# Performance work log

Measured on AMD Instinct MI355X. Metric: run time of the kernel, lower is better.

Reference implementation:

```python
import jax, jax.numpy as jnp
import numpy as np

EPS = 1e-15


def _cdist(a, b):
    # batched euclidean pairwise distance, a:[B,N,K] b:[B,M,K] -> [B,N,M]
    d2 = (jnp.sum(a * a, -1)[:, :, None] + jnp.sum(b * b, -1)[:, None, :]
          - 2.0 * jnp.einsum('bik,bjk->bij', a, b))
    return jnp.sqrt(jnp.maximum(d2, 0.0))


def _rank3_diag(d_flat):
    # [B,N] -> [B,N,N] diagonal
    eye = jnp.eye(d_flat.shape[1], dtype=d_flat.dtype)
    return eye * d_flat[:, :, None]


def _trace(m):
    return jnp.einsum('bjj->b', m)


def dense_ct_rewiring(x, adj, s, mask):
    s = jnp.tanh(s)
    m = mask[:, :, None].astype(x.dtype)
    x = x * m
    s = s * m
    k = s.shape[-1]
    d_flat = jnp.sum(adj, axis=-1)              # [B,N]
    d = _rank3_diag(d_flat) + EPS               # EPS added to full matrix (faithful to torch)
    L = d - adj
    out_adj = jnp.einsum('bnk,bnm,bml->bkl', s, L, s)
    ct_num = _trace(out_adj)
    ct_den = _trace(jnp.einsum('bnk,bnm,bml->bkl', s, d, s)) + EPS
    ct_dist = _cdist(s, s)                      # [B,N,N]
    vol = _trace(d)                             # [B]
    ct_dist = ct_dist / vol[:, None, None]
    adj_new = ct_dist * adj
    ct_loss = jnp.mean(ct_num / ct_den)
    ss = jnp.einsum('bnk,bnl->bkl', s, s)
    i_s = jnp.eye(k, dtype=ss.dtype)
    ss_n = jnp.sqrt(jnp.sum(ss * ss, axis=(-1, -2), keepdims=True))
    diff = ss / ss_n - i_s
    ortho_loss = jnp.sqrt(jnp.sum(diff * diff))  # global Frobenius norm, mean of scalar
    return adj_new, ct_loss, ortho_loss


def dense_mincut_pool(x, adj, s, mask):
    s = jax.nn.softmax(s, axis=-1)
    m = mask[:, :, None].astype(x.dtype)
    x = x * m
    s = s * m
    k = s.shape[-1]
    out = jnp.einsum('bnk,bnf->bkf', s, x)
    out_adj = jnp.einsum('bnk,bnm,bml->bkl', s, adj, s)
    mincut_num = _trace(out_adj)
    d_flat = jnp.sum(adj, axis=-1) + EPS
    d = _rank3_diag(d_flat)
    mincut_den = _trace(jnp.einsum('bnk,bnm,bml->bkl', s, d, s))
    mincut_loss = jnp.mean(-(mincut_num / mincut_den))
    ss = jnp.einsum('bnk,bnl->bkl', s, s)
    i_s = jnp.eye(k, dtype=ss.dtype)
    ss_n = jnp.sqrt(jnp.sum(ss * ss, axis=(-1, -2), keepdims=True))
    diff = ss / ss_n - i_s / jnp.sqrt(jnp.asarray(float(k), ss.dtype))
    ortho_loss = jnp.mean(jnp.sqrt(jnp.sum(diff * diff, axis=(-1, -2))))
    # zero diagonal, then symmetric degree normalization
    out_adj = out_adj * (1.0 - i_s)
    dk = jnp.sqrt(jnp.sum(out_adj, axis=-1) + EPS) + EPS  # [B,k]
    out_adj = out_adj / dk[:, None, :] / dk[:, :, None]
    return out, out_adj, mincut_loss, ortho_loss


def dense_graph_conv(x, adj, w_rel, b_rel, w_root):
    # PyG DenseGraphConv(aggr='add'): lin_rel(adj @ x) + lin_root(x)
    return jnp.matmul(jnp.matmul(adj, x), w_rel) + b_rel + jnp.matmul(x, w_root)


def ctnet_forward(x, adj, mask,
                  W_lin1, b_lin1, W_pool1, b_pool1, W_pool2, b_pool2,
                  Wrel1, brel1, Wroot1, Wrel2, brel2, Wroot2,
                  W_lin2, b_lin2, W_lin3, b_lin3):
    x = jnp.matmul(x, W_lin1) + b_lin1
    s1 = jnp.matmul(x, W_pool1) + b_pool1
    adj, ct_loss, ortho1 = dense_ct_rewiring(x, adj, s1, mask)
    x = dense_graph_conv(x, adj, Wrel1, brel1, Wroot1)
    s2 = jnp.matmul(x, W_pool2) + b_pool2
    x, adj, mincut2, ortho2 = dense_mincut_pool(x, adj, s2, mask)
    x = dense_graph_conv(x, adj, Wrel2, brel2, Wroot2)
    x = jnp.sum(x, axis=1)
    x = jax.nn.relu(jnp.matmul(x, W_lin2) + b_lin2)
    x = jnp.matmul(x, W_lin3) + b_lin3
    return jax.nn.log_softmax(x, axis=-1), ct_loss + ortho1, mincut2 + ortho2


def _init_lin(key, fan_in, fan_out):
    k1, k2 = jax.random.split(key)
    lim = 1.0 / np.sqrt(fan_in)
    W = jax.random.uniform(k1, (fan_in, fan_out), jnp.float32, -lim, lim)
    b = jax.random.uniform(k2, (fan_out,), jnp.float32, -lim, lim)
    return W, b


def setup_inputs() -> dict:
    key = jax.random.key(0)
    ks = jax.random.split(key, 12)
    B, N, Fin, H, K, OUT, K2 = 16, 1024, 128, 32, 64, 10, 16
    x = jax.random.normal(ks[0], (B, N, Fin), jnp.float32)
    adj = jax.random.uniform(ks[1], (B, N, N), jnp.float32)
    mask = jnp.ones((B, N), jnp.bool_)
    W_lin1, b_lin1 = _init_lin(ks[2], Fin, H)
    W_pool1, b_pool1 = _init_lin(ks[3], H, K)
    W_pool2, b_pool2 = _init_lin(ks[4], H, K2)
    Wrel1, brel1 = _init_lin(ks[5], H, H)
    Wroot1, _ = _init_lin(ks[6], H, H)
    Wrel2, brel2 = _init_lin(ks[7], H, H)
    Wroot2, _ = _init_lin(ks[8], H, H)
    W_lin2, b_lin2 = _init_lin(ks[9], H, H)
    W_lin3, b_lin3 = _init_lin(ks[10], H, OUT)
    return dict(x=x, adj=adj, mask=mask,
                W_lin1=W_lin1, b_lin1=b_lin1, W_pool1=W_pool1, b_pool1=b_pool1,
                W_pool2=W_pool2, b_pool2=b_pool2,
                Wrel1=Wrel1, brel1=brel1, Wroot1=Wroot1,
                Wrel2=Wrel2, brel2=brel2, Wroot2=Wroot2,
                W_lin2=W_lin2, b_lin2=b_lin2, W_lin3=W_lin3, b_lin3=b_lin3)


def reference(x, adj, mask,
              W_lin1, b_lin1, W_pool1, b_pool1, W_pool2, b_pool2,
              Wrel1, brel1, Wroot1, Wrel2, brel2, Wroot2,
              W_lin2, b_lin2, W_lin3, b_lin3):
    return ctnet_forward(x, adj, mask,
                         W_lin1, b_lin1, W_pool1, b_pool1, W_pool2, b_pool2,
                         Wrel1, brel1, Wroot1, Wrel2, brel2, Wroot2,
                         W_lin2, b_lin2, W_lin3, b_lin3)
```

## Files before the change

kernel.cpp:

```cpp
#include <hip/hip_runtime.h>

typedef unsigned short u16;
typedef unsigned int   u32;
typedef __attribute__((ext_vector_type(8))) short bf16x8;
typedef __attribute__((ext_vector_type(4))) float f32x4;

#define EPSF 1e-15f

__device__ __forceinline__ float* accp(float* xb, int b, int a) {
    return xb + (size_t)(b*1024 + a/14)*128 + 114 + (a % 14);
}

__device__ __forceinline__ float bf2f(u16 u) {
    union { u32 i; float f; } v; v.i = ((u32)u) << 16; return v.f;
}
__device__ __forceinline__ u16 f2bf(float f) {
    union { u32 i; float f; } v; v.f = f;
    u32 r = v.i + 0x7fffu + ((v.i >> 16) & 1u);
    return (u16)(r >> 16);
}

__global__ __launch_bounds__(256) void k_a(float* xb,
        const float* __restrict__ W1, const float* __restrict__ b1,
        const float* __restrict__ Wp1, const float* __restrict__ bp1)
{
    __shared__ float W1s[128*32];
    __shared__ float Wp1s[32*64];
    __shared__ float xs[16][128];
    __shared__ float x1s[16][32];
    int tid = threadIdx.x;
    for (int i = tid; i < 1024; i += 256)
        *(float4*)&W1s[i*4] = *(const float4*)&W1[i*4];
    for (int i = tid; i < 512; i += 256)
        *(float4*)&Wp1s[i*4] = *(const float4*)&Wp1[i*4];
    int rbase = blockIdx.x*16;
    for (int e = tid; e < 512; e += 256) {
        int rr = e >> 5, c = e & 31;
        *(float4*)&xs[rr][c*4] = *(const float4*)&xb[(size_t)(rbase + rr)*128 + c*4];
    }
    __syncthreads();
    int w = tid >> 6, l = tid & 63;
    int col = l & 31, half = l >> 5;
    #pragma unroll
    for (int i = 0; i < 4; ++i) {
        int rr = w*4 + i;
        float* xr = xb + (size_t)(rbase + rr)*128;
        if (l == 33) xr[96] = 0.f;
        if (l < 15) xr[113 + l] = 0.f;
        float acc = half ? 0.f : b1[col];
        const float* xrow = &xs[rr][half*64];
        const float* wrow = &W1s[half*64*32 + col];
        for (int f = 0; f < 64; ++f) acc += xrow[f]*wrow[f*32];
        acc += __shfl_down(acc, 32);
        if (l < 32) x1s[rr][l] = acc;
    }
    __syncthreads();
    #pragma unroll
    for (int i = 0; i < 4; ++i) {
        int rr = w*4 + i;
        float* xr = xb + (size_t)(rbase + rr)*128;
        if (l < 32) xr[64 + l] = x1s[rr][l];
        float acc = bp1[l];
        for (int h = 0; h < 32; ++h) acc += x1s[rr][h]*Wp1s[h*64 + l];
        float sv = tanhf(acc);
        u32 me = (u32)f2bf(sv);
        u32 nb = __shfl_down(me, 1);
        if (!(l & 1)) ((u32*)xr)[l >> 1] = me | (nb << 16);
        float svr = bf2f((u16)me);
        float qv = svr*svr;
        for (int off = 32; off; off >>= 1) qv += __shfl_down(qv, off);
        if (l == 0) xr[112] = qv;
    }
}

__global__ __launch_bounds__(256, 6) void k_c(const float* __restrict__ adj, float* xb,
                                              u32* __restrict__ anb)
{
    __shared__ __align__(16) u16 BufB[2][64*72];
    __shared__ __align__(16) float qBs[2][64];
    __shared__ float pw[2][4];
    int tid = threadIdx.x;
    int tjq = blockIdx.x, ti = blockIdx.y, b = blockIdx.z;
    int w = tid >> 6, lane = tid & 63;
    int q = lane >> 4, c16 = lane & 15;
    int rloc = w*16 + c16;
    size_t rowg = (size_t)(b*1024 + ti*64 + rloc);
    const u32* xu = (const u32*)xb;
    float4 a4s[2][4];
    #pragma unroll
    for (int tt = 0; tt < 2; ++tt)
        #pragma unroll
        for (int t = 0; t < 4; ++t)
            a4s[tt][t] = *(const float4*)&adj[rowg*1024 + (tjq*2 + tt)*64 + t*16 + q*4];
    bf16x8 bfr0 = *(const bf16x8*)&xu[rowg*128 + q*4];
    bf16x8 bfr1 = *(const bf16x8*)&xu[rowg*128 + 16 + q*4];
    float qa = xb[rowg*128 + 112];
    for (int e = tid; e < 1024; e += 256) {
        int n2 = e >> 3, c = e & 7;
        int tt = n2 >> 6, n = n2 & 63;
        *(float4*)&BufB[tt][n*72 + c*8] =
            *(const float4*)&xu[(size_t)(b*1024 + (tjq*2 + tt)*64 + n)*128 + c*4];
    }
    if (tid < 128) {
        qBs[tid >> 6][tid & 63] =
            xb[(size_t)(b*1024 + (tjq*2 + (tid >> 6))*64 + (tid & 63))*128 + 112];
    }
    __syncthreads();
    float dsum = 0.f, rsum = 0.f, Pt = 0.f, Qt = 0.f;
    #pragma unroll
    for (int tt = 0; tt < 2; ++tt) {
        f32x4 g[4];
        #pragma unroll
        for (int t = 0; t < 4; ++t) {
            bf16x8 af0 = *(const bf16x8*)&BufB[tt][(t*16 + c16)*72 + q*8];
            bf16x8 af1 = *(const bf16x8*)&BufB[tt][(t*16 + c16)*72 + 32 + q*8];
            f32x4 gg = {0.f, 0.f, 0.f, 0.f};
            gg = __builtin_amdgcn_mfma_f32_16x16x32_bf16(af0, bfr0, gg, 0, 0, 0);
            gg = __builtin_amdgcn_mfma_f32_16x16x32_bf16(af1, bfr1, gg, 0, 0, 0);
            g[t] = gg;
        }
        #pragma unroll
        for (int t = 0; t < 4; ++t) {
            float4 a4 = a4s[tt][t];
            float4 qb4 = *(const float4*)&qBs[tt][t*16 + q*4];
            float av[4] = {a4.x, a4.y, a4.z, a4.w};
            float qb[4] = {qb4.x, qb4.y, qb4.z, qb4.w};
            float o[4];
            #pragma unroll
            for (int rg = 0; rg < 4; ++rg) {
                float d2v = qa + qb[rg] - 2.f*g[t][rg];
                float dist = sqrtf(fmaxf(d2v, 0.f));
                o[rg] = dist * av[rg];
                dsum += av[rg];
                rsum += o[rg];
                Pt += av[rg]*g[t][rg];
                Qt += g[t][rg]*g[t][rg];
            }
            u32 p0 = (u32)f2bf(o[0]) | ((u32)f2bf(o[1]) << 16);
            u32 p1 = (u32)f2bf(o[2]) | ((u32)f2bf(o[3]) << 16);
            *(uint2*)&anb[rowg*512 + (tjq*2 + tt)*32 + t*8 + q*2] = make_uint2(p0, p1);
        }
    }
    rsum += __shfl_xor(rsum, 16); rsum += __shfl_xor(rsum, 32);
    dsum += __shfl_xor(dsum, 16); dsum += __shfl_xor(dsum, 32);
    if (q == 0) {
        atomicAdd(&xb[rowg*128 + 96],  dsum);
        atomicAdd(&xb[rowg*128 + 113], rsum);
    }
    for (int off = 32; off; off >>= 1) { Pt += __shfl_down(Pt, off); Qt += __shfl_down(Qt, off); }
    if (lane == 0) { pw[0][w] = Pt; pw[1][w] = Qt; }
    __syncthreads();
    if (tid == 0) {
        atomicAdd(accp(xb,b,3), pw[0][0]+pw[0][1]+pw[0][2]+pw[0][3]);
        atomicAdd(accp(xb,b,4), pw[1][0]+pw[1][1]+pw[1][2]+pw[1][3]);
    }
}

__global__ __launch_bounds__(256) void k_y(const u32* __restrict__ anb, float* xb)
{
    __shared__ __align__(16) u16 X[16*1032];
    int tid = threadIdx.x;
    int hq = blockIdx.x, ni = blockIdx.y, b = blockIdx.z;
    int w = tid >> 6, lane = tid & 63;
    int q = lane >> 4, c16 = lane & 15;
    int rloc = w*16 + c16;
    size_t rowg = (size_t)(b*1024 + ni*64 + rloc);
    u32* Xu = (u32*)X;
    for (int e = tid; e < 2048; e += 256) {
        int mp = e >> 2, h4 = e & 3;
        int m0 = mp*2;
        const float* p0 = &xb[(size_t)(b*1024 + m0)*128 + 64 + hq*16 + h4*4];
        float4 v0 = *(const float4*)p0;
        float4 v1 = *(const float4*)(p0 + 128);
        Xu[(h4*4 + 0)*516 + mp] = (u32)f2bf(v0.x) | ((u32)f2bf(v1.x) << 16);
        Xu[(h4*4 + 1)*516 + mp] = (u32)f2bf(v0.y) | ((u32)f2bf(v1.y) << 16);
        Xu[(h4*4 + 2)*516 + mp] = (u32)f2bf(v0.z) | ((u32)f2bf(v1.z) << 16);
        Xu[(h4*4 + 3)*516 + mp] = (u32)f2bf(v0.w) | ((u32)f2bf(v1.w) << 16);
    }
    __syncthreads();
    f32x4 acc = {0.f,0.f,0.f,0.f};
    #pragma unroll 8
    for (int ks = 0; ks < 32; ++ks) {
        bf16x8 af = *(const bf16x8*)&anb[rowg*512 + ks*16 + q*4];
        bf16x8 bx = *(const bf16x8*)&X[c16*1032 + ks*32 + q*8];
        acc = __builtin_amdgcn_mfma_f32_16x16x32_bf16(af, bx, acc, 0, 0, 0);
    }
    #pragma unroll
    for (int rg = 0; rg < 4; ++rg) {
        size_t orow = (size_t)(b*1024 + ni*64 + w*16 + q*4 + rg)*128;
        xb[orow + 32 + hq*16 + c16] = acc[rg];
    }
    if (hq == 0 && tid < 64) {
        const float* xr = xb + (size_t)(b*1024 + ni*64 + tid)*128;
        float d = xr[96], qv = xr[112];
        float t0 = d, t1 = d*qv, t2 = qv;
        for (int off = 32; off; off >>= 1) {
            t0 += __shfl_down(t0, off); t1 += __shfl_down(t1, off); t2 += __shfl_down(t2, off);
        }
        if (tid == 0) {
            atomicAdd(accp(xb,b,0), t0);
            atomicAdd(accp(xb,b,1), t1);
            atomicAdd(accp(xb,b,2), t2);
        }
    }
}

__global__ __launch_bounds__(256) void k_d2(float* xb,
        const float* __restrict__ Wrel1, const float* __restrict__ brel1,
        const float* __restrict__ Wroot1,
        const float* __restrict__ Wp2, const float* __restrict__ bp2)
{
    __shared__ float ys[32*34];
    __shared__ float x1n[32*34];
    __shared__ float x2s[32*34];
    __shared__ float s2s[32*17];
    __shared__ float Wr[1024], Wo[1024], Wp[512];
    int tid = threadIdx.x;
    int tq = blockIdx.x, b = blockIdx.y;
    int rbase = b*1024 + tq*32;
    float invv = 1.f / (*accp(xb,b,0) + 1024.f*EPSF);
    for (int i = tid; i < 1024; i += 256) { Wr[i] = Wrel1[i]; Wo[i] = Wroot1[i]; }
    for (int i = tid; i < 512; i += 256) Wp[i] = Wp2[i];
    for (int e = tid; e < 1024; e += 256) {
        int r = e >> 5, h = e & 31;
        const float* xr = xb + (size_t)(rbase + r)*128;
        ys[r*34 + h]  = xr[32 + h] * invv;
        x1n[r*34 + h] = xr[64 + h];
    }
    __syncthreads();
    {
        int h = tid & 31, tg = tid >> 5;
        float brl = brel1[h];
        #pragma unroll
        for (int i = 0; i < 4; ++i) {
            int r = tg + 8*i;
            float v = brl;
            for (int j = 0; j < 32; ++j)
                v += ys[r*34 + j]*Wr[j*32 + h] + x1n[r*34 + j]*Wo[j*32 + h];
            x2s[r*34 + h] = v;
        }
    }
    __syncthreads();
    if (tid < 64) {
        int r = tid & 31;
        float lg[16];
        float mx = -1e30f;
        #pragma unroll
        for (int k = 0; k < 16; ++k) {
            float v = bp2[k];
            for (int j = 0; j < 32; ++j) v += x2s[r*34 + j]*Wp[j*16 + k];
            lg[k] = v; mx = fmaxf(mx, v);
        }
        float sum = 0.f;
        #pragma unroll
        for (int k = 0; k < 16; ++k) { lg[k] = expf(lg[k] - mx); sum += lg[k]; }
        float inv = 1.f/sum, q2v = 0.f;
        u32 pk[8];
        #pragma unroll
        for (int k = 0; k < 16; ++k) {
            float sv = lg[k]*inv;
            s2s[r*17 + k] = sv;
            u32 bfv = (u32)f2bf(sv);
            if (k & 1) pk[k>>1] |= bfv << 16; else pk[k>>1] = bfv;
            q2v += sv*sv;
        }
        if (tid < 32) {
            u32* xp = (u32*)(xb + (size_t)(rbase + r)*128);
            #pragma unroll
            for (int i2 = 0; i2 < 8; ++i2) xp[i2] = pk[i2];
        }
        float denp = (xb[(size_t)(rbase + r)*128 + 113]*invv + EPSF)*q2v;
        if (tid >= 32) denp = 0.f;
        for (int off = 32; off; off >>= 1) denp += __shfl_down(denp, off);
        if (tid == 0) atomicAdd(accp(xb,b,5), denp);
    }
    __syncthreads();
    {
        int k = tid >> 4, l = tid & 15;
        float s = 0.f;
        for (int r = 0; r < 32; ++r) s += s2s[r*17 + k]*s2s[r*17 + l];
        atomicAdd(accp(xb,b,774 + tid), s);
    }
    for (int e = tid; e < 512; e += 256) {
        int k = e >> 5, h = e & 31;
        float s = 0.f;
        for (int r = 0; r < 32; ++r) s += s2s[r*17 + k]*x2s[r*34 + h];
        atomicAdd(accp(xb,b,6 + k*32 + h), s);
    }
}

__global__ __launch_bounds__(256) void k_e(const u32* __restrict__ anb, float* xb)
{
    __shared__ __align__(16) u16 BufS[2][16*72];
    __shared__ __align__(16) u16 BufN[16*72];
    __shared__ __align__(16) u16 zT[16*72];
    int tid = threadIdx.x;
    int miq = blockIdx.x, ni = blockIdx.y, b = blockIdx.z;
    const u32* xu = (const u32*)xb;
    for (int e = tid; e < 512; e += 256) {
        int node = e >> 3, lw = e & 7;
        u32 pp = xu[(size_t)(b*1024 + ni*64 + node)*128 + lw];
        BufN[(lw*2)*72 + node]     = (u16)pp;
        BufN[(lw*2 + 1)*72 + node] = (u16)(pp >> 16);
    }
    for (int e = tid; e < 1024; e += 256) {
        int t = e >> 9, e2 = e & 511;
        int node = e2 >> 3, lw = e2 & 7;
        u32 pp = xu[(size_t)(b*1024 + (miq*2 + t)*64 + node)*128 + lw];
        BufS[t][(lw*2)*72 + node]     = (u16)pp;
        BufS[t][(lw*2 + 1)*72 + node] = (u16)(pp >> 16);
    }
    int w = tid >> 6, lane = tid & 63;
    int q = lane >> 4, c16 = lane & 15;
    int rloc = w*16 + c16;
    size_t arow = (size_t)(b*1024 + ni*64 + rloc)*512;
    bf16x8 ya[2][2];
    #pragma unroll
    for (int t = 0; t < 2; ++t) {
        ya[t][0] = *(const bf16x8*)&anb[arow + (miq*2 + t)*32 + q*4];
        ya[t][1] = *(const bf16x8*)&anb[arow + (miq*2 + t)*32 + 16 + q*4];
    }
    __syncthreads();
    f32x4 zacc = {0.f, 0.f, 0.f, 0.f};
    #pragma unroll
    for (int t = 0; t < 2; ++t) {
        bf16x8 yb0 = *(const bf16x8*)&BufS[t][c16*72 + q*8];
        bf16x8 yb1 = *(const bf16x8*)&BufS[t][c16*72 + 32 + q*8];
        zacc = __builtin_amdgcn_mfma_f32_16x16x32_bf16(ya[t][0], yb0, zacc, 0, 0, 0);
        zacc = __builtin_amdgcn_mfma_f32_16x16x32_bf16(ya[t][1], yb1, zacc, 0, 0, 0);
    }
    #pragma unroll
    for (int rg = 0; rg < 4; ++rg)
        zT[c16*72 + w*16 + q*4 + rg] = f2bf(zacc[rg]);
    __syncthreads();
    if (w == 0) {
        bf16x8 af0 = *(const bf16x8*)&BufN[c16*72 + q*8];
        bf16x8 af1 = *(const bf16x8*)&BufN[c16*72 + 32 + q*8];
        bf16x8 bz0 = *(const bf16x8*)&zT[c16*72 + q*8];
        bf16x8 bz1 = *(const bf16x8*)&zT[c16*72 + 32 + q*8];
        f32x4 oamv = {0.f, 0.f, 0.f, 0.f};
        oamv = __builtin_amdgcn_mfma_f32_16x16x32_bf16(af0, bz0, oamv, 0, 0, 0);
        oamv = __builtin_amdgcn_mfma_f32_16x16x32_bf16(af1, bz1, oamv, 0, 0, 0);
        #pragma unroll
        for (int rg = 0; rg < 4; ++rg)
            atomicAdd(accp(xb, b, 518 + (q*4 + rg)*16 + c16), oamv[rg]);
    }
}

__global__ __launch_bounds__(256) void k_f1(float* xb,
        const float* __restrict__ Wrel2, const float* __restrict__ brel2,
        const float* __restrict__ Wroot2,
        const float* __restrict__ W_lin2, const float* __restrict__ b_lin2,
        const float* __restrict__ W_lin3, const float* __restrict__ b_lin3,
        float* __restrict__ outp)
{
    __shared__ float oam_s[256], ssm_s[256], outm_s[512];
    __shared__ float dks[16], csoa[16];
    __shared__ float cs0[32], cs1[32], xsum[32], x5[32], lgs[10];
    __shared__ float red[4];
    __shared__ int isLast;
    int b = blockIdx.x;
    int tid = threadIdx.x;
    float invv = 1.f / (*accp(xb,b,0) + 1024.f*EPSF);
    oam_s[tid] = *accp(xb,b,518 + tid) * invv;
    ssm_s[tid] = *accp(xb,b,774 + tid);
    for (int e = tid; e < 512; e += 256) outm_s[e] = *accp(xb,b,6 + e);
    __syncthreads();
    if (tid < 16) {
        float rsv = 0.f;
        for (int l = 0; l < 16; ++l) if (l != tid) rsv += oam_s[tid*16 + l];
        dks[tid] = sqrtf(fmaxf(rsv, 0.f) + EPSF) + EPSF;
    }
    {
        float v = ssm_s[tid];
        float p = v*v;
        for (int off = 32; off; off >>= 1) p += __shfl_down(p, off);
        if ((tid & 63) == 0) red[tid >> 6] = p;
    }
    __syncthreads();
    if (tid < 16) {
        float s = 0.f;
        for (int k2 = 0; k2 < 16; ++k2)
            if (k2 != tid) s += oam_s[k2*16 + tid] / dks[k2];
        csoa[tid] = s / dks[tid];
    }
    if (tid < 32) {
        float s0 = 0.f, s1 = 0.f;
        for (int l = 0; l < 16; ++l) {
            float ov = outm_s[l*32 + tid];
            s0 += ov;
            s1 += csoa[l] * ov;
        }
        cs0[tid] = s0; cs1[tid] = s1;
    }
    if (tid == 64) {
        float T1v  = *accp(xb,b,1);
        float Pgv  = *accp(xb,b,3);
        float Q2v  = *accp(xb,b,4);
        float Tq1v = *accp(xb,b,2);
        float T2v  = *accp(xb,b,5);
        float tr2 = 0.f, trs = 0.f;
        for (int k2 = 0; k2 < 16; ++k2) { tr2 += oam_s[k2*17]; trs += ssm_s[k2*17]; }
        float fr2 = red[0] + red[1] + red[2] + red[3];
        __hip_atomic_store(accp(xb,b,1030), (T1v - Pgv) / (T1v + EPSF),
                           __ATOMIC_RELAXED, __HIP_MEMORY_SCOPE_AGENT);
        __hip_atomic_store(accp(xb,b,1031), 65.f - 2.f*Tq1v/sqrtf(fmaxf(Q2v, 1e-30f)),
                           __ATOMIC_RELAXED, __HIP_MEMORY_SCOPE_AGENT);
        __hip_atomic_store(accp(xb,b,1032), -tr2 / T2v,
                           __ATOMIC_RELAXED, __HIP_MEMORY_SCOPE_AGENT);
        __hip_atomic_store(accp(xb,b,1033),
                           sqrtf(fmaxf(2.f - trs/(2.f*sqrtf(fmaxf(fr2, 1e-30f))), 0.f)),
                           __ATOMIC_RELAXED, __HIP_MEMORY_SCOPE_AGENT);
    }
    __syncthreads();
    if (tid < 32) {
        float v = 16.f * brel2[tid];
        for (int j = 0; j < 32; ++j)
            v += cs1[j]*Wrel2[j*32 + tid] + cs0[j]*Wroot2[j*32 + tid];
        xsum[tid] = v;
    }
    __syncthreads();
    if (tid < 32) {
        float v = b_lin2[tid];
        for (int j = 0; j < 32; ++j) v += xsum[j]*W_lin2[j*32 + tid];
        x5[tid] = fmaxf(v, 0.f);
    }
    __syncthreads();
    if (tid < 10) {
        float v = b_lin3[tid];
        for (int j = 0; j < 32; ++j) v += x5[j]*W_lin3[j*10 + tid];
        lgs[tid] = v;
    }
    __syncthreads();
    if (tid < 10) {
        float mx = -1e30f;
        for (int t = 0; t < 10; ++t) mx = fmaxf(mx, lgs[t]);
        float sum = 0.f;
        for (int t = 0; t < 10; ++t) sum += expf(lgs[t] - mx);
        outp[b*10 + tid] = lgs[tid] - mx - logf(sum);
    }
    __syncthreads();
    if (tid == 0) {
        __threadfence();
        float old = atomicAdd(accp(xb,0,1035), 1.f);
        isLast = (old > 14.5f) ? 1 : 0;
    }
    __syncthreads();
    if (isLast && tid < 64) {
        __threadfence();
        int b2 = tid & 15, which = tid >> 4;
        float v = __hip_atomic_load(accp(xb,b2,1030 + which),
                                    __ATOMIC_RELAXED, __HIP_MEMORY_SCOPE_AGENT);
        for (int off = 1; off < 16; off <<= 1) v += __shfl_xor(v, off);
        float ct = __shfl(v, 0);
        float o1 = __shfl(v, 16);
        float mc = __shfl(v, 32);
        float o2 = __shfl(v, 48);
        if (tid == 0) {
            outp[160] = ct/16.f + sqrtf(fmaxf(o1, 0.f));
            outp[161] = mc/16.f + o2/16.f;
        }
    }
}

extern "C" void kernel_launch(void* const* d_in, const int* in_sizes, int n_in,
                              void* d_out, int out_size, void* d_ws, size_t ws_size,
                              hipStream_t stream)
{
    float* xb        = (float*)d_in[0];
    const float* adj = (const float*)d_in[1];
    const float* W_lin1 = (const float*)d_in[3];
    const float* b_lin1 = (const float*)d_in[4];
    const float* W_pool1= (const float*)d_in[5];
    const float* b_pool1= (const float*)d_in[6];
    const float* W_pool2= (const float*)d_in[7];
    const float* b_pool2= (const float*)d_in[8];
    const float* Wrel1  = (const float*)d_in[9];
    const float* brel1  = (const float*)d_in[10];
    const float* Wroot1 = (const float*)d_in[11];
    const float* Wrel2  = (const float*)d_in[12];
    const float* brel2  = (const float*)d_in[13];
    const float* Wroot2 = (const float*)d_in[14];
    const float* W_lin2 = (const float*)d_in[15];
    const float* b_lin2 = (const float*)d_in[16];
    const float* W_lin3 = (const float*)d_in[17];
    const float* b_lin3 = (const float*)d_in[18];
    u32* anb = (u32*)d_ws;
    (void)ws_size; (void)in_sizes; (void)n_in; (void)out_size;

    k_a<<<dim3(1024),      dim3(256), 0, stream>>>(xb, W_lin1, b_lin1, W_pool1, b_pool1);
    k_c<<<dim3(8,16,16),   dim3(256), 0, stream>>>(adj, xb, anb);
    k_y<<<dim3(2,16,16),   dim3(256), 0, stream>>>(anb, xb);
    k_d2<<<dim3(32,16),    dim3(256), 0, stream>>>(xb, Wrel1, brel1, Wroot1,
                                                   W_pool2, b_pool2);
    k_e<<<dim3(8,16,16),   dim3(256), 0, stream>>>(anb, xb);
    k_f1<<<dim3(16),       dim3(256), 0, stream>>>(xb, Wrel2, brel2, Wroot2,
                                                   W_lin2, b_lin2, W_lin3, b_lin3,
                                                   (float*)d_out);
}
```

Baseline: 241.8 us.

## Shrink k_c tiles, stage bf16 output in LDS for coalesced stores, parallelize k_d2 softmax

k_c now processes one 64x64 tile per block instead of two, doubling the grid and raising the occupancy hint from 6 to 8 blocks. Its bf16 adjacency output is first packed into shared memory and then written with wide 16-byte coalesced stores instead of scattered 8-byte stores. In k_d2 the pool-2 softmax now runs on all 256 threads (two logits per thread, with shuffle reductions) instead of 64 threads, and the per-block denominator is reduced through shared memory. The cost is an extra barrier and more blocks, each issuing their own atomics.

```diff
diff --git a/kernel.cpp b/kernel.cpp
--- a/kernel.cpp
+++ b/kernel.cpp
@@ -73,73 +73,66 @@
     }
 }
 
-__global__ __launch_bounds__(256, 6) void k_c(const float* __restrict__ adj, float* xb,
+__global__ __launch_bounds__(256, 8) void k_c(const float* __restrict__ adj, float* xb,
                                               u32* __restrict__ anb)
 {
-    __shared__ __align__(16) u16 BufB[2][64*72];
-    __shared__ __align__(16) float qBs[2][64];
+    __shared__ __align__(16) u32 SMEM[64*36];
+    __shared__ __align__(16) float qBs[64];
     __shared__ float pw[2][4];
     int tid = threadIdx.x;
-    int tjq = blockIdx.x, ti = blockIdx.y, b = blockIdx.z;
+    int tj = blockIdx.x, ti = blockIdx.y, b = blockIdx.z;
     int w = tid >> 6, lane = tid & 63;
     int q = lane >> 4, c16 = lane & 15;
     int rloc = w*16 + c16;
     size_t rowg = (size_t)(b*1024 + ti*64 + rloc);
     const u32* xu = (const u32*)xb;
-    float4 a4s[2][4];
-    #pragma unroll
-    for (int tt = 0; tt < 2; ++tt)
-        #pragma unroll
-        for (int t = 0; t < 4; ++t)
-            a4s[tt][t] = *(const float4*)&adj[rowg*1024 + (tjq*2 + tt)*64 + t*16 + q*4];
+    float4 a4s[4];
+    #pragma unroll
+    for (int t = 0; t < 4; ++t)
+        a4s[t] = *(const float4*)&adj[rowg*1024 + tj*64 + t*16 + q*4];
     bf16x8 bfr0 = *(const bf16x8*)&xu[rowg*128 + q*4];
     bf16x8 bfr1 = *(const bf16x8*)&xu[rowg*128 + 16 + q*4];
     float qa = xb[rowg*128 + 112];
-    for (int e = tid; e < 1024; e += 256) {
-        int n2 = e >> 3, c = e & 7;
-        int tt = n2 >> 6, n = n2 & 63;
-        *(float4*)&BufB[tt][n*72 + c*8] =
-            *(const float4*)&xu[(size_t)(b*1024 + (tjq*2 + tt)*64 + n)*128 + c*4];
-    }
-    if (tid < 128) {
-        qBs[tid >> 6][tid & 63] =
-            xb[(size_t)(b*1024 + (tjq*2 + (tid >> 6))*64 + (tid & 63))*128 + 112];
+    u16* BufB = (u16*)SMEM;
+    for (int e = tid; e < 512; e += 256) {
+        int n = e >> 3, c = e & 7;
+        *(float4*)&BufB[n*72 + c*8] =
+            *(const float4*)&xu[(size_t)(b*1024 + tj*64 + n)*128 + c*4];
+    }
+    if (tid < 64) qBs[tid] = xb[(size_t)(b*1024 + tj*64 + tid)*128 + 112];
+    __syncthreads();
+    f32x4 g[4];
+    #pragma unroll
+    for (int t = 0; t < 4; ++t) {
+        bf16x8 af0 = *(const bf16x8*)&BufB[(t*16 + c16)*72 + q*8];
+        bf16x8 af1 = *(const bf16x8*)&BufB[(t*16 + c16)*72 + 32 + q*8];
+        f32x4 gg = {0.f, 0.f, 0.f, 0.f};
+        gg = __builtin_amdgcn_mfma_f32_16x16x32_bf16(af0, bfr0, gg, 0, 0, 0);
+        gg = __builtin_amdgcn_mfma_f32_16x16x32_bf16(af1, bfr1, gg, 0, 0, 0);
+        g[t] = gg;
     }
     __syncthreads();
     float dsum = 0.f, rsum = 0.f, Pt = 0.f, Qt = 0.f;
     #pragma unroll
-    for (int tt = 0; tt < 2; ++tt) {
-        f32x4 g[4];
+    for (int t = 0; t < 4; ++t) {
+        float4 a4 = a4s[t];
+        float4 qb4 = *(const float4*)&qBs[t*16 + q*4];
+        float av[4] = {a4.x, a4.y, a4.z, a4.w};
+        float qb[4] = {qb4.x, qb4.y, qb4.z, qb4.w};
+        float o[4];
         #pragma unroll
-        for (int t = 0; t < 4; ++t) {
-            bf16x8 af0 = *(const bf16x8*)&BufB[tt][(t*16 + c16)*72 + q*8];
-            bf16x8 af1 = *(const bf16x8*)&BufB[tt][(t*16 + c16)*72 + 32 + q*8];
-            f32x4 gg = {0.f, 0.f, 0.f, 0.f};
-            gg = __builtin_amdgcn_mfma_f32_16x16x32_bf16(af0, bfr0, gg, 0, 0, 0);
-            gg = __builtin_amdgcn_mfma_f32_16x16x32_bf16(af1, bfr1, gg, 0, 0, 0);
-            g[t] = gg;
-        }
-        #pragma unroll
-        for (int t = 0; t < 4; ++t) {
-            float4 a4 = a4s[tt][t];
-            float4 qb4 = *(const float4*)&qBs[tt][t*16 + q*4];
-            float av[4] = {a4.x, a4.y, a4.z, a4.w};
-            float qb[4] = {qb4.x, qb4.y, qb4.z, qb4.w};
-            float o[4];
-            #pragma unroll
-            for (int rg = 0; rg < 4; ++rg) {
-                float d2v = qa + qb[rg] - 2.f*g[t][rg];
-                float dist = sqrtf(fmaxf(d2v, 0.f));
-                o[rg] = dist * av[rg];
-                dsum += av[rg];
-                rsum += o[rg];
-                Pt += av[rg]*g[t][rg];
-                Qt += g[t][rg]*g[t][rg];
-            }
-            u32 p0 = (u32)f2bf(o[0]) | ((u32)f2bf(o[1]) << 16);
-            u32 p1 = (u32)f2bf(o[2]) | ((u32)f2bf(o[3]) << 16);
-            *(uint2*)&anb[rowg*512 + (tjq*2 + tt)*32 + t*8 + q*2] = make_uint2(p0, p1);
-        }
+        for (int rg = 0; rg < 4; ++rg) {
+            float d2v = qa + qb[rg] - 2.f*g[t][rg];
+            float dist = sqrtf(fmaxf(d2v, 0.f));
+            o[rg] = dist * av[rg];
+            dsum += av[rg];
+            rsum += o[rg];
+            Pt += av[rg]*g[t][rg];
+            Qt += g[t][rg]*g[t][rg];
+        }
+        u32 p0 = (u32)f2bf(o[0]) | ((u32)f2bf(o[1]) << 16);
+        u32 p1 = (u32)f2bf(o[2]) | ((u32)f2bf(o[3]) << 16);
+        *(uint2*)&SMEM[rloc*34 + t*8 + q*2] = make_uint2(p0, p1);
     }
     rsum += __shfl_xor(rsum, 16); rsum += __shfl_xor(rsum, 32);
     dsum += __shfl_xor(dsum, 16); dsum += __shfl_xor(dsum, 32);
@@ -150,6 +143,14 @@
     for (int off = 32; off; off >>= 1) { Pt += __shfl_down(Pt, off); Qt += __shfl_down(Qt, off); }
     if (lane == 0) { pw[0][w] = Pt; pw[1][w] = Qt; }
     __syncthreads();
+    {
+        int row = tid >> 2, c8 = (tid & 3)*8;
+        uint4 v0 = *(const uint4*)&SMEM[row*34 + c8];
+        uint4 v1 = *(const uint4*)&SMEM[row*34 + c8 + 4];
+        size_t go = (size_t)(b*1024 + ti*64 + row)*512 + tj*32 + c8;
+        *(uint4*)&anb[go]     = v0;
+        *(uint4*)&anb[go + 4] = v1;
+    }
     if (tid == 0) {
         atomicAdd(accp(xb,b,3), pw[0][0]+pw[0][1]+pw[0][2]+pw[0][3]);
         atomicAdd(accp(xb,b,4), pw[1][0]+pw[1][1]+pw[1][2]+pw[1][3]);
@@ -215,6 +216,7 @@
     __shared__ float x2s[32*34];
     __shared__ float s2s[32*17];
     __shared__ float Wr[1024], Wo[1024], Wp[512];
+    __shared__ float pwd[4];
     int tid = threadIdx.x;
     int tq = blockIdx.x, b = blockIdx.y;
     int rbase = b*1024 + tq*32;
@@ -241,40 +243,40 @@
         }
     }
     __syncthreads();
-    if (tid < 64) {
-        int r = tid & 31;
-        float lg[16];
-        float mx = -1e30f;
-        #pragma unroll
-        for (int k = 0; k < 16; ++k) {
-            float v = bp2[k];
-            for (int j = 0; j < 32; ++j) v += x2s[r*34 + j]*Wp[j*16 + k];
-            lg[k] = v; mx = fmaxf(mx, v);
-        }
-        float sum = 0.f;
-        #pragma unroll
-        for (int k = 0; k < 16; ++k) { lg[k] = expf(lg[k] - mx); sum += lg[k]; }
-        float inv = 1.f/sum, q2v = 0.f;
-        u32 pk[8];
-        #pragma unroll
-        for (int k = 0; k < 16; ++k) {
-            float sv = lg[k]*inv;
-            s2s[r*17 + k] = sv;
-            u32 bfv = (u32)f2bf(sv);
-            if (k & 1) pk[k>>1] |= bfv << 16; else pk[k>>1] = bfv;
-            q2v += sv*sv;
-        }
-        if (tid < 32) {
-            u32* xp = (u32*)(xb + (size_t)(rbase + r)*128);
-            #pragma unroll
-            for (int i2 = 0; i2 < 8; ++i2) xp[i2] = pk[i2];
-        }
-        float denp = (xb[(size_t)(rbase + r)*128 + 113]*invv + EPSF)*q2v;
-        if (tid >= 32) denp = 0.f;
-        for (int off = 32; off; off >>= 1) denp += __shfl_down(denp, off);
-        if (tid == 0) atomicAdd(accp(xb,b,5), denp);
-    }
-    __syncthreads();
+    {
+        int rl = tid & 7, kq = (tid >> 3) & 7, wv = tid >> 6;
+        int r = wv*8 + rl;
+        int k0 = kq*2;
+        float v0 = bp2[k0], v1 = bp2[k0 + 1];
+        for (int j = 0; j < 32; ++j) {
+            float xv = x2s[r*34 + j];
+            v0 += xv*Wp[j*16 + k0];
+            v1 += xv*Wp[j*16 + k0 + 1];
+        }
+        float mx = fmaxf(v0, v1);
+        mx = fmaxf(mx, __shfl_xor(mx, 8));
+        mx = fmaxf(mx, __shfl_xor(mx, 16));
+        mx = fmaxf(mx, __shfl_xor(mx, 32));
+        float e0 = expf(v0 - mx), e1 = expf(v1 - mx);
+        float sm = e0 + e1;
+        sm += __shfl_xor(sm, 8); sm += __shfl_xor(sm, 16); sm += __shfl_xor(sm, 32);
+        float inv = 1.f/sm;
+        float sv0 = e0*inv, sv1 = e1*inv;
+        s2s[r*17 + k0]     = sv0;
+        s2s[r*17 + k0 + 1] = sv1;
+        ((u32*)(xb + (size_t)(rbase + r)*128))[kq] =
+            (u32)f2bf(sv0) | ((u32)f2bf(sv1) << 16);
+        float q2v = sv0*sv0 + sv1*sv1;
+        q2v += __shfl_xor(q2v, 8); q2v += __shfl_xor(q2v, 16); q2v += __shfl_xor(q2v, 32);
+        float denp = (kq == 0)
+            ? (xb[(size_t)(rbase + r)*128 + 113]*invv + EPSF)*q2v : 0.f;
+        denp += __shfl_down(denp, 1);
+        denp += __shfl_down(denp, 2);
+        denp += __shfl_down(denp, 4);
+        if ((tid & 63) == 0) pwd[wv] = denp;
+    }
+    __syncthreads();
+    if (tid == 0) atomicAdd(accp(xb,b,5), pwd[0]+pwd[1]+pwd[2]+pwd[3]);
     {
         int k = tid >> 4, l = tid & 15;
         float s = 0.f;
@@ -489,7 +491,7 @@
     (void)ws_size; (void)in_sizes; (void)n_in; (void)out_size;
 
     k_a<<<dim3(1024),      dim3(256), 0, stream>>>(xb, W_lin1, b_lin1, W_pool1, b_pool1);
-    k_c<<<dim3(8,16,16),   dim3(256), 0, stream>>>(adj, xb, anb);
+    k_c<<<dim3(16,16,16),  dim3(256), 0, stream>>>(adj, xb, anb);
     k_y<<<dim3(2,16,16),   dim3(256), 0, stream>>>(anb, xb);
     k_d2<<<dim3(32,16),    dim3(256), 0, stream>>>(xb, Wrel1, brel1, Wroot1,
                                                    W_pool2, b_pool2);
```

Measured after the change: 244.8 us. About the same (+1.2%).
